# Kernel tuning notes

Measured on AMD Instinct MI355X. Metric: run time of the kernel, lower is better.

The kernel has to match this reference:

```python
import jax, jax.numpy as jnp
import numpy as np

B, K, NP = 2, 48, 25            # batch, context_length, grid_x*grid_y
C, H, L = 768, 12, 6            # n_embd, n_head, n_layer
COLORS, VOCAB, IS = 10, 40, 26  # color_num, vocab_size, intention_size
MAXT = 1000                     # max_timestep
TOK = NP + 4                    # tokens per timestep (rtg, 25 states, action, pnp, intention)
T = K * TOK                     # total sequence length


def layernorm(x, g, b, eps=1e-5):
    m = x.mean(-1, keepdims=True)
    v = ((x - m) ** 2).mean(-1, keepdims=True)
    return (x - m) * jax.lax.rsqrt(v + eps) * g + b


def causal_attn(x, wq, bq, wk, bk, wv, bv, wo, bo):
    Bx, Tx, Cx = x.shape
    hd = Cx // H
    def heads(w, bb):
        return (x @ w + bb).reshape(Bx, Tx, H, hd).transpose(0, 2, 1, 3)
    q, k, v = heads(wq, bq), heads(wk, bk), heads(wv, bv)
    att = jnp.einsum('bhqd,bhkd->bhqk', q, k) * (1.0 / np.sqrt(hd))
    mask = jnp.tril(jnp.ones((Tx, Tx), bool))
    att = jnp.where(mask, att, -jnp.inf)
    att = jax.nn.softmax(att, axis=-1)
    y = jnp.einsum('bhqk,bhkd->bhqd', att, v).transpose(0, 2, 1, 3).reshape(Bx, Tx, Cx)
    return y @ wo + bo


def setup_inputs() -> dict:
    key = jax.random.key(0)
    ks = iter(jax.random.split(key, 64))
    def nrm(shape):
        return jax.random.normal(next(ks), shape, jnp.float32) * 0.02
    inp = dict(
        states=jax.random.randint(next(ks), (B, K * NP), 0, COLORS),
        actions=jax.random.randint(next(ks), (B, K), 0, VOCAB),
        rtgs=jax.random.normal(next(ks), (B, K), jnp.float32),
        timesteps=jax.random.randint(next(ks), (B, K), 0, MAXT + 1),
        pnp=jax.random.normal(next(ks), (B, K, NP), jnp.float32),
        intentions=jax.random.randint(next(ks), (B, K, 2), 0, IS),
        pos_emb=nrm((K + 1, C)),               # (block_size, C)
        global_pos_emb=nrm((MAXT + 1, C)),
        state_tab=nrm((COLORS, C)),
        action_tab=nrm((VOCAB, C)),
        ret_W=nrm((1, C)), ret_b=jnp.zeros((C,)),
        pnp_W=nrm((NP, C)), pnp_b=jnp.zeros((C,)),
        src_tab=nrm((IS, C)), dst_tab=nrm((IS, C)),
        int_W=nrm((2 * C, C)), int_b=jnp.zeros((C,)),
        ln1_g=jnp.ones((L, C)), ln1_b=jnp.zeros((L, C)),
        ln2_g=jnp.ones((L, C)), ln2_b=jnp.zeros((L, C)),
        Wq=nrm((L, C, C)), bq=jnp.zeros((L, C)),
        Wk=nrm((L, C, C)), bk=jnp.zeros((L, C)),
        Wv=nrm((L, C, C)), bv=jnp.zeros((L, C)),
        Wo=nrm((L, C, C)), bo=jnp.zeros((L, C)),
        Wm1=nrm((L, C, 4 * C)), bm1=jnp.zeros((L, 4 * C)),
        Wm2=nrm((L, 4 * C, C)), bm2=jnp.zeros((L, C)),
        lnf_g=jnp.ones((C,)), lnf_b=jnp.zeros((C,)),
        Whs=nrm((C, COLORS)), bhs=jnp.zeros((COLORS,)),
        Wha=nrm((C, VOCAB)), bha=jnp.zeros((VOCAB,)),
        Whr=nrm((C, 1)), bhr=jnp.zeros((1,)),
        Whi=nrm((C, 2 * IS)), bhi=jnp.zeros((2 * IS,)),
    )
    return inp


def reference(states, actions, rtgs, timesteps, pnp, intentions,
              pos_emb, global_pos_emb, state_tab, action_tab,
              ret_W, ret_b, pnp_W, pnp_b, src_tab, dst_tab, int_W, int_b,
              ln1_g, ln1_b, ln2_g, ln2_b, Wq, bq, Wk, bk, Wv, bv, Wo, bo,
              Wm1, bm1, Wm2, bm2, lnf_g, lnf_b,
              Whs, bhs, Wha, bha, Whr, bhr, Whi, bhi):
    # --- embeddings, interleaved as [rtg, state_0..24, action, pnp, intention] per timestep ---
    st = state_tab[states].reshape(B, K, NP, C)                    # strided writes 1+i::TOK
    ae = action_tab[actions][:, :, None, :]
    re = (rtgs[..., None] @ ret_W + ret_b)[:, :, None, :]          # rtgs.unsqueeze(-1) -> Linear(1,C)
    pe = (pnp @ pnp_W + pnp_b)[:, :, None, :]
    ie_in = jnp.concatenate([src_tab[intentions[..., 0]], dst_tab[intentions[..., 1]]], axis=-1)
    ie = (ie_in @ int_W + int_b)[:, :, None, :]
    tok = jnp.concatenate([re, st, ae, pe, ie], axis=2).reshape(B, T, C)
    # --- positions: gather global + local pos_emb[:block_size-1], repeat_interleave by TOK ---
    pos = global_pos_emb[timesteps] + pos_emb[:K][None]            # (B, K, C)
    x = tok + jnp.repeat(pos, TOK, axis=1)
    # --- transformer stack (dropout p=0) ---
    def blk(h, p):
        l1g, l1b, l2g, l2b, wq, bq_, wk, bk_, wv, bv_, wo, bo_, w1, b1, w2, b2 = p
        h = h + causal_attn(layernorm(h, l1g, l1b), wq, bq_, wk, bk_, wv, bv_, wo, bo_)
        m = layernorm(h, l2g, l2b)
        h = h + jax.nn.gelu(m @ w1 + b1, approximate=False) @ w2 + b2
        return h, None
    x, _ = jax.lax.scan(blk, x, (ln1_g, ln1_b, ln2_g, ln2_b, Wq, bq, Wk, bk, Wv, bv, Wo, bo, Wm1, bm1, Wm2, bm2))
    x = layernorm(x, lnf_g, lnf_b)
    xr = x.reshape(B, K, TOK, C)
    logits = x @ Whs + bhs                                         # (B, T, COLORS)
    logit_action = xr[:, :, NP + 1] @ Wha + bha                    # (B, K, VOCAB)
    logit_rtg = (xr[:, :, 0] @ Whr + bhr)[..., 0]                  # (B, K)
    li = xr[:, :, NP + 3] @ Whi + bhi                              # (B, K, 2*IS)
    return logits, logit_action, logit_rtg, li[..., :IS], li[..., IS:]
```

## Files before the change

kernel.cpp:

```cpp
#include <hip/hip_runtime.h>
#include <hip/hip_bf16.h>
#include <math.h>


typedef __hip_bfloat16 bf16;
typedef __attribute__((ext_vector_type(4))) short s4v;
typedef __attribute__((ext_vector_type(8))) short s8v;
typedef __attribute__((ext_vector_type(4))) float f4v;
typedef unsigned int u32;

#define DEV static __device__ __forceinline__

constexpr int NBATCH = 2;
constexpr int NK   = 48;
constexpr int NNP  = 25;
constexpr int NC   = 768;
constexpr int NH   = 12;
constexpr int NL   = 6;
constexpr int NTOK = 29;
constexpr int NT   = NK * NTOK;
constexpr int NM   = NBATCH * NT;
constexpr int MPAD = 2816;

DEV float bs2f(short s) {
  unsigned u = ((unsigned)(unsigned short)s) << 16;
  float f; __builtin_memcpy(&f, &u, 4); return f;
}
DEV short f2bs(float f) {
  bf16 h = __float2bfloat16(f);
  short s; __builtin_memcpy(&s, &h, 2); return s;
}

DEV void async16(const short* g, short* l) {
  __builtin_amdgcn_global_load_lds(
      (const __attribute__((address_space(1))) u32*)g,
      (__attribute__((address_space(3))) u32*)l, 16, 0, 0);
}

__global__ __launch_bounds__(256) void transpose_kernel(
    const float* __restrict__ src, bf16* __restrict__ dst, int R, int C)
{
  int c0 = blockIdx.x * 32, r0 = blockIdx.y * 32;
  __shared__ float tl[32][33];
  int rr = threadIdx.x >> 5, cc = threadIdx.x & 31;
#pragma unroll
  for (int p = 0; p < 4; p++)
    tl[rr + p * 8][cc] = src[(long)(r0 + rr + p * 8) * C + c0 + cc];
  __syncthreads();
#pragma unroll
  for (int p = 0; p < 4; p++)
    dst[(long)(c0 + rr + p * 8) * R + r0 + cc] = __float2bfloat16(tl[cc][rr + p * 8]);
}

__global__ __launch_bounds__(256) void transpose_layer_kernel(
    const float* __restrict__ Wq, const float* __restrict__ Wk,
    const float* __restrict__ Wv, const float* __restrict__ Wo,
    const float* __restrict__ Wm1, const float* __restrict__ Wm2,
    bf16* __restrict__ WqkvT, bf16* __restrict__ WoT,
    bf16* __restrict__ Wm1T, bf16* __restrict__ Wm2T, int multi)
{
  int blk = blockIdx.x;
  int l = blk / 6912, t = blk - l * 6912;
  long so = (long)l * 768 * 768;
  long mo = (long)l * 768 * 3072;
  long dl = multi ? l : 0;
  const float* src; bf16* dst; int R, C, tile;
  if (t < 1728) {
    int m = t / 576; tile = t - m * 576;
    src = (m == 0 ? Wq : (m == 1 ? Wk : Wv)) + so;
    dst = WqkvT + dl * (2304L * 768) + (long)m * 768 * 768; R = 768; C = 768;
  } else if (t < 2304) { src = Wo + so;  dst = WoT  + dl * (768L * 768);  tile = t - 1728; R = 768;  C = 768;  }
  else if (t < 4608)   { src = Wm1 + mo; dst = Wm1T + dl * (3072L * 768); tile = t - 2304; R = 768;  C = 3072; }
  else                 { src = Wm2 + mo; dst = Wm2T + dl * (768L * 3072); tile = t - 4608; R = 3072; C = 768;  }
  int ct = C / 32;
  int tr = tile / ct, tc = tile - tr * ct;
  int r0 = tr * 32, c0 = tc * 32;
  __shared__ float tl[32][33];
  int rr = threadIdx.x >> 5, cc = threadIdx.x & 31;
#pragma unroll
  for (int p = 0; p < 4; p++)
    tl[rr + p * 8][cc] = src[(long)(r0 + rr + p * 8) * C + c0 + cc];
  __syncthreads();
#pragma unroll
  for (int p = 0; p < 4; p++)
    dst[(long)(c0 + rr + p * 8) * R + r0 + cc] = __float2bfloat16(tl[cc][rr + p * 8]);
}

__global__ __launch_bounds__(256) void gather_ie_kernel(
    const int* __restrict__ intentions, const float* __restrict__ src_tab,
    const float* __restrict__ dst_tab, bf16* __restrict__ ie_in)
{
  int idx = blockIdx.x * 256 + threadIdx.x;
  if (idx >= 96 * 1536) return;
  int row = idx / 1536, col = idx - row * 1536;
  float v;
  if (col < 768) v = src_tab[intentions[row * 2 + 0] * 768 + col];
  else           v = dst_tab[intentions[row * 2 + 1] * 768 + col - 768];
  ie_in[idx] = __float2bfloat16(v);
}

__global__ __launch_bounds__(256) void embed_kernel(
    const int* __restrict__ states, const int* __restrict__ actions,
    const float* __restrict__ rtgs, const int* __restrict__ timesteps,
    const float* __restrict__ pnp,
    const float* __restrict__ pos_emb, const float* __restrict__ gpe,
    const float* __restrict__ state_tab, const float* __restrict__ action_tab,
    const float* __restrict__ retW, const float* __restrict__ retb,
    const float* __restrict__ pnpW, const float* __restrict__ pnpb,
    const bf16* __restrict__ ieb, float* __restrict__ X)
{
  int bk = blockIdx.x;
  int b = bk / NK, ts = bk - b * NK;
  int c = blockIdx.y * 256 + threadIdx.x;

  float rtg = rtgs[bk];
  int tstep = timesteps[bk];
  int act   = actions[bk];

  long base = (long)(b * NT + ts * NTOK) * NC;
  float pos = gpe[(long)tstep * NC + c] + pos_emb[ts * NC + c];

  X[base + c] = rtg * retW[c] + retb[c] + pos;
  const int* sp = states + bk * NNP;
#pragma unroll
  for (int i = 0; i < NNP; i++)
    X[base + (1 + i) * NC + c] = state_tab[sp[i] * NC + c] + pos;
  X[base + 26 * NC + c] = action_tab[act * NC + c] + pos;
  float ap = pnpb[c];
  const float* pv = pnp + bk * NNP;
#pragma unroll
  for (int i = 0; i < NNP; i++) ap += pv[i] * pnpW[i * NC + c];
  X[base + 27 * NC + c] = ap + pos;
  X[base + 28 * NC + c] = __bfloat162float(ieb[bk * NC + c]) + pos;
}

__global__ __launch_bounds__(256) void ln_kernel(
    const float* __restrict__ X, bf16* __restrict__ XN,
    const float* __restrict__ g, const float* __restrict__ bt)
{
  int row = blockIdx.x, tid = threadIdx.x;
  const float* x = X + (long)row * NC;
  float v0 = x[tid], v1 = x[tid + 256], v2 = x[tid + 512];
  float s = v0 + v1 + v2;
#pragma unroll
  for (int o = 32; o > 0; o >>= 1) s += __shfl_down(s, o, 64);
  __shared__ float red[8];
  if ((tid & 63) == 0) red[tid >> 6] = s;
  __syncthreads();
  float mean = (red[0] + red[1] + red[2] + red[3]) * (1.0f / NC);
  float d0 = v0 - mean, d1 = v1 - mean, d2 = v2 - mean;
  float qq = d0 * d0 + d1 * d1 + d2 * d2;
#pragma unroll
  for (int o = 32; o > 0; o >>= 1) qq += __shfl_down(qq, o, 64);
  __syncthreads();
  if ((tid & 63) == 0) red[tid >> 6] = qq;
  __syncthreads();
  float var = (red[0] + red[1] + red[2] + red[3]) * (1.0f / NC);
  float rs = 1.0f / sqrtf(var + 1e-5f);
  bf16* xn = XN + (long)row * NC;
  xn[tid      ] = __float2bfloat16(d0 * rs * g[tid      ] + bt[tid      ]);
  xn[tid + 256] = __float2bfloat16(d1 * rs * g[tid + 256] + bt[tid + 256]);
  xn[tid + 512] = __float2bfloat16(d2 * rs * g[tid + 512] + bt[tid + 512]);
}

template<int BM>
__global__ __launch_bounds__(256) void gemm_kernel(
    const bf16* __restrict__ A, const bf16* __restrict__ WT,
    const float* __restrict__ b0, const float* __restrict__ b1,
    const float* __restrict__ b2, int Nsplit,
    bf16* __restrict__ outb, float* __restrict__ resid,
    int M, int N, int K, int flags)
{
  constexpr int IM  = BM / 64;
  constexpr int ACH = BM / 64;
  __shared__ __align__(1024) short As[2][BM * 32];
  __shared__ __align__(1024) short Bs[2][64 * 32];

  int tid = threadIdx.x, wave = tid >> 6, lane = tid & 63;
  int quad = lane >> 4, l16 = lane & 15;
  int m0 = blockIdx.y * BM, n0 = blockIdx.x * 64;
  int wm = wave * (BM / 4);
  int lr = lane >> 2, lc = (lane & 3) * 8;

  const short* Ag = (const short*)A + (long)m0 * K + lc;
  const short* Bg = (const short*)WT + (long)n0 * K + lc;

  const short* ag[ACH]; int alo[ACH];
#pragma unroll
  for (int c = 0; c < ACH; c++) {
    int rbase = wave * (16 * ACH) + c * 16;
    ag[c] = Ag + (long)(rbase + lr) * K;
    alo[c] = rbase * 32;
  }
  const short* bg = Bg + (long)(wave * 16 + lr) * K;
  int blo = wave * 16 * 32;

  f4v zero4 = {0.f, 0.f, 0.f, 0.f};
  f4v acc[IM][4];
#pragma unroll
  for (int i = 0; i < IM; i++)
#pragma unroll
    for (int j = 0; j < 4; j++) acc[i][j] = zero4;

  int nk = K >> 5;
#pragma unroll
  for (int c = 0; c < ACH; c++) async16(ag[c], &As[0][alo[c]]);
  async16(bg, &Bs[0][blo]);
  __syncthreads();

  for (int kt = 0; kt < nk; kt++) {
    int cur = kt & 1, nxt = cur ^ 1;
    if (kt + 1 < nk) {
      int ko = (kt + 1) << 5;
#pragma unroll
      for (int c = 0; c < ACH; c++) async16(ag[c] + ko, &As[nxt][alo[c]]);
      async16(bg + ko, &Bs[nxt][blo]);
    }
    s8v af[IM], bf8[4];
#pragma unroll
    for (int i = 0; i < IM; i++) {
      const short* p = &As[cur][(wm + i * 16 + l16) * 32 + quad * 8];
      af[i].lo = *(const s4v*)p; af[i].hi = *(const s4v*)(p + 4);
    }
#pragma unroll
    for (int j = 0; j < 4; j++) {
      const short* p = &Bs[cur][(j * 16 + l16) * 32 + quad * 8];
      bf8[j].lo = *(const s4v*)p; bf8[j].hi = *(const s4v*)(p + 4);
    }
#pragma unroll
    for (int i = 0; i < IM; i++)
#pragma unroll
      for (int j = 0; j < 4; j++)
        acc[i][j] = __builtin_amdgcn_mfma_f32_16x16x32_bf16(af[i], bf8[j], acc[i][j], 0, 0, 0);
    __syncthreads();
  }

#pragma unroll
  for (int i = 0; i < IM; i++) {
    int rbase = m0 + wm + i * 16 + quad * 4;
#pragma unroll
    for (int j = 0; j < 4; j++) {
      int bc = n0 + j * 16;
      int wsel = bc / Nsplit;
      const float* bp = wsel == 0 ? b0 : (wsel == 1 ? b1 : b2);
      float bv = bp[bc - wsel * Nsplit + l16];
      int col = bc + l16;
#pragma unroll
      for (int r = 0; r < 4; r++) {
        int row = rbase + r;
        if (row < M) {
          float v = acc[i][j][r] + bv;
          if (flags & 1) v = 0.5f * v * (1.0f + erff(v * 0.70710678118654752f));
          if (flags & 2) resid[(long)row * N + col] += v;
          else outb[(long)row * N + col] = __float2bfloat16(v);
        }
      }
    }
  }
}

constexpr int ASTR = 72;

__global__ __launch_bounds__(256) void attn_kernel(
    const bf16* __restrict__ QKV, bf16* __restrict__ Yg)
{
  int qt = blockIdx.x, h = blockIdx.y, b = blockIdx.z;
  int q0 = qt * 64;
  int tid = threadIdx.x, wave = tid >> 6, lane = tid & 63, quad = lane >> 4, l16 = lane & 15;

  __shared__ short Qs[64 * ASTR];
  __shared__ short Ks[64 * ASTR];
  __shared__ short Vt[64 * ASTR];
  __shared__ short Ps[64 * ASTR];
  __shared__ float S[64 * 65];
  __shared__ float mrow[64], lrow[64], arow[64];
  __shared__ float red[256];

  if (tid < 64) { mrow[tid] = -1e30f; lrow[tid] = 0.f; }

  int r = tid >> 2, c16 = (tid & 3) * 16;
  const short* src = (const short*)QKV;
  s8v zz = {0,0,0,0,0,0,0,0};

  s8v qv0 = zz, qv1 = zz;
  if (q0 + r < NT) {
    const s8v* p = (const s8v*)(src + (long)(b * NT + q0 + r) * 2304 + h * 64 + c16);
    qv0 = p[0]; qv1 = p[1];
  }
  {
    short* qp = &Qs[r * ASTR + c16];
    *(s4v*)(qp    ) = qv0.lo; *(s4v*)(qp + 4) = qv0.hi;
    *(s4v*)(qp + 8) = qv1.lo; *(s4v*)(qp + 12) = qv1.hi;
  }

  f4v zero4 = {0.f, 0.f, 0.f, 0.f};
  f4v Of[4];
#pragma unroll
  for (int j = 0; j < 4; j++) Of[j] = zero4;

  int kend = q0 + 63; if (kend > NT - 1) kend = NT - 1;
  for (int k0 = 0; k0 <= kend; k0 += 64) {
    s8v kv0 = zz, kv1 = zz, vv0 = zz, vv1 = zz;
    if (k0 + r < NT) {
      const s8v* pk = (const s8v*)(src + (long)(b * NT + k0 + r) * 2304 + 768 + h * 64 + c16);
      kv0 = pk[0]; kv1 = pk[1];
      const s8v* pvv = (const s8v*)(src + (long)(b * NT + k0 + r) * 2304 + 1536 + h * 64 + c16);
      vv0 = pvv[0]; vv1 = pvv[1];
    }
    __syncthreads();
    {
      short* kp = &Ks[r * ASTR + c16];
      *(s4v*)(kp    ) = kv0.lo; *(s4v*)(kp + 4) = kv0.hi;
      *(s4v*)(kp + 8) = kv1.lo; *(s4v*)(kp + 12) = kv1.hi;
      short* vt = &Vt[c16 * ASTR + r];
      vt[ 0 * ASTR] = vv0.s0; vt[ 1 * ASTR] = vv0.s1; vt[ 2 * ASTR] = vv0.s2; vt[ 3 * ASTR] = vv0.s3;
      vt[ 4 * ASTR] = vv0.s4; vt[ 5 * ASTR] = vv0.s5; vt[ 6 * ASTR] = vv0.s6; vt[ 7 * ASTR] = vv0.s7;
      vt[ 8 * ASTR] = vv1.s0; vt[ 9 * ASTR] = vv1.s1; vt[10 * ASTR] = vv1.s2; vt[11 * ASTR] = vv1.s3;
      vt[12 * ASTR] = vv1.s4; vt[13 * ASTR] = vv1.s5; vt[14 * ASTR] = vv1.s6; vt[15 * ASTR] = vv1.s7;
    }
    __syncthreads();

    f4v sa[4];
#pragma unroll
    for (int j = 0; j < 4; j++) sa[j] = zero4;
#pragma unroll
    for (int ks = 0; ks < 2; ks++) {
      const short* pa = &Qs[(wave * 16 + l16) * ASTR + ks * 32 + quad * 8];
      s8v aq; aq.lo = *(const s4v*)pa; aq.hi = *(const s4v*)(pa + 4);
#pragma unroll
      for (int j = 0; j < 4; j++) {
        const short* pb = &Ks[(j * 16 + l16) * ASTR + ks * 32 + quad * 8];
        s8v bk8; bk8.lo = *(const s4v*)pb; bk8.hi = *(const s4v*)(pb + 4);
        sa[j] = __builtin_amdgcn_mfma_f32_16x16x32_bf16(aq, bk8, sa[j], 0, 0, 0);
      }
    }
#pragma unroll
    for (int j = 0; j < 4; j++) {
#pragma unroll
      for (int rg = 0; rg < 4; rg++) {
        int rloc = wave * 16 + quad * 4 + rg;
        int cloc = j * 16 + l16;
        int gq = q0 + rloc, gk = k0 + cloc;
        float sv = (gk <= gq && gq < NT) ? sa[j][rg] * 0.125f : -1e30f;
        S[rloc * 65 + cloc] = sv;
      }
    }
    __syncthreads();

    float mx = -1e30f;
#pragma unroll
    for (int c = 0; c < 16; c++) mx = fmaxf(mx, S[r * 65 + c16 + c]);
    red[r * 4 + (tid & 3)] = mx;
    __syncthreads();
    if (tid < 64) {
      float tm = fmaxf(fmaxf(red[tid * 4], red[tid * 4 + 1]), fmaxf(red[tid * 4 + 2], red[tid * 4 + 3]));
      float mn = fmaxf(mrow[tid], tm);
      arow[tid] = __expf(mrow[tid] - mn);
      mrow[tid] = mn;
    }
    __syncthreads();

    float mr = mrow[r];
    float psum = 0.f;
#pragma unroll
    for (int c = 0; c < 16; c++) {
      float e = __expf(S[r * 65 + c16 + c] - mr);
      psum += e;
      Ps[r * ASTR + c16 + c] = f2bs(e);
    }
    red[r * 4 + (tid & 3)] = psum;
    __syncthreads();
    if (tid < 64)
      lrow[tid] = lrow[tid] * arow[tid] + red[tid * 4] + red[tid * 4 + 1] + red[tid * 4 + 2] + red[tid * 4 + 3];
#pragma unroll
    for (int j = 0; j < 4; j++)
#pragma unroll
      for (int rg = 0; rg < 4; rg++)
        Of[j][rg] *= arow[wave * 16 + quad * 4 + rg];
    __syncthreads();

#pragma unroll
    for (int ks = 0; ks < 2; ks++) {
      const short* pa = &Ps[(wave * 16 + l16) * ASTR + ks * 32 + quad * 8];
      s8v ap8; ap8.lo = *(const s4v*)pa; ap8.hi = *(const s4v*)(pa + 4);
#pragma unroll
      for (int j = 0; j < 4; j++) {
        const short* pb = &Vt[(j * 16 + l16) * ASTR + ks * 32 + quad * 8];
        s8v vp8; vp8.lo = *(const s4v*)pb; vp8.hi = *(const s4v*)(pb + 4);
        Of[j] = __builtin_amdgcn_mfma_f32_16x16x32_bf16(ap8, vp8, Of[j], 0, 0, 0);
      }
    }
  }
  __syncthreads();
#pragma unroll
  for (int j = 0; j < 4; j++) {
#pragma unroll
    for (int rg = 0; rg < 4; rg++) {
      int rloc = wave * 16 + quad * 4 + rg;
      int gq = q0 + rloc;
      if (gq < NT) {
        float ov = Of[j][rg] / lrow[rloc];
        Yg[(long)(b * NT + gq) * NC + h * 64 + j * 16 + l16] = __float2bfloat16(ov);
      }
    }
  }
}

__global__ __launch_bounds__(256) void head_logits_kernel(
    const bf16* __restrict__ XN, const float* __restrict__ Whs,
    const float* __restrict__ bhs, float* __restrict__ out)
{
  int idx = blockIdx.x * 256 + threadIdx.x;
  if (idx >= NM * 10) return;
  int row = idx / 10, n = idx - row * 10;
  const short* x = (const short*)XN + (long)row * NC;
  float a0 = bhs[n], a1 = 0.f, a2 = 0.f, a3 = 0.f;
  for (int k = 0; k < NC; k += 4) {
    a0 += bs2f(x[k    ]) * Whs[(k    ) * 10 + n];
    a1 += bs2f(x[k + 1]) * Whs[(k + 1) * 10 + n];
    a2 += bs2f(x[k + 2]) * Whs[(k + 2) * 10 + n];
    a3 += bs2f(x[k + 3]) * Whs[(k + 3) * 10 + n];
  }
  out[idx] = a0 + a1 + a2 + a3;
}

__global__ __launch_bounds__(128) void head_small_kernel(
    const bf16* __restrict__ XN,
    const float* __restrict__ Wha, const float* __restrict__ bha,
    const float* __restrict__ Whr, const float* __restrict__ bhr,
    const float* __restrict__ Whi, const float* __restrict__ bhi,
    float* __restrict__ outA, float* __restrict__ outR,
    float* __restrict__ outS, float* __restrict__ outD)
{
  int blk = blockIdx.x;
  int b = blk / NK, ts = blk - b * NK;
  int tid = threadIdx.x;
  if (tid >= 93) return;
  const short* xs = (const short*)XN;
  if (tid < 40) {
    long row = (long)(b * NT + ts * NTOK + 26) * NC;
    float a0 = bha[tid], a1 = 0.f, a2 = 0.f, a3 = 0.f;
    for (int k = 0; k < NC; k += 4) {
      a0 += bs2f(xs[row + k    ]) * Wha[(k    ) * 40 + tid];
      a1 += bs2f(xs[row + k + 1]) * Wha[(k + 1) * 40 + tid];
      a2 += bs2f(xs[row + k + 2]) * Wha[(k + 2) * 40 + tid];
      a3 += bs2f(xs[row + k + 3]) * Wha[(k + 3) * 40 + tid];
    }
    outA[blk * 40 + tid] = a0 + a1 + a2 + a3;
  } else if (tid == 40) {
    long row = (long)(b * NT + ts * NTOK) * NC;
    float a0 = bhr[0], a1 = 0.f, a2 = 0.f, a3 = 0.f;
    for (int k = 0; k < NC; k += 4) {
      a0 += bs2f(xs[row + k    ]) * Whr[k    ];
      a1 += bs2f(xs[row + k + 1]) * Whr[k + 1];
      a2 += bs2f(xs[row + k + 2]) * Whr[k + 2];
      a3 += bs2f(xs[row + k + 3]) * Whr[k + 3];
    }
    outR[blk] = a0 + a1 + a2 + a3;
  } else {
    int n = tid - 41;
    long row = (long)(b * NT + ts * NTOK + 28) * NC;
    float a0 = bhi[n], a1 = 0.f, a2 = 0.f, a3 = 0.f;
    for (int k = 0; k < NC; k += 4) {
      a0 += bs2f(xs[row + k    ]) * Whi[(k    ) * 52 + n];
      a1 += bs2f(xs[row + k + 1]) * Whi[(k + 1) * 52 + n];
      a2 += bs2f(xs[row + k + 2]) * Whi[(k + 2) * 52 + n];
      a3 += bs2f(xs[row + k + 3]) * Whi[(k + 3) * 52 + n];
    }
    if (n < 26) outS[blk * 26 + n] = a0 + a1 + a2 + a3;
    else        outD[blk * 26 + (n - 26)] = a0 + a1 + a2 + a3;
  }
}

extern "C" void kernel_launch(void* const* d_in, const int* in_sizes, int n_in,
                              void* d_out, int out_size, void* d_ws, size_t ws_size,
                              hipStream_t stream)
{
  (void)in_sizes; (void)n_in; (void)out_size;

  const int*   states     = (const int*)  d_in[0];
  const int*   actions    = (const int*)  d_in[1];
  const float* rtgs       = (const float*)d_in[2];
  const int*   timesteps  = (const int*)  d_in[3];
  const float* pnp        = (const float*)d_in[4];
  const int*   intentions = (const int*)  d_in[5];
  const float* pos_emb    = (const float*)d_in[6];
  const float* gpe        = (const float*)d_in[7];
  const float* state_tab  = (const float*)d_in[8];
  const float* action_tab = (const float*)d_in[9];
  const float* retW  = (const float*)d_in[10];
  const float* retb  = (const float*)d_in[11];
  const float* pnpW  = (const float*)d_in[12];
  const float* pnpb  = (const float*)d_in[13];
  const float* src_tab = (const float*)d_in[14];
  const float* dst_tab = (const float*)d_in[15];
  const float* intW  = (const float*)d_in[16];
  const float* intb  = (const float*)d_in[17];
  const float* ln1g  = (const float*)d_in[18];
  const float* ln1b  = (const float*)d_in[19];
  const float* ln2g  = (const float*)d_in[20];
  const float* ln2b  = (const float*)d_in[21];
  const float* Wq = (const float*)d_in[22];
  const float* bq = (const float*)d_in[23];
  const float* Wk = (const float*)d_in[24];
  const float* bk = (const float*)d_in[25];
  const float* Wv = (const float*)d_in[26];
  const float* bv = (const float*)d_in[27];
  const float* Wo = (const float*)d_in[28];
  const float* bo = (const float*)d_in[29];
  const float* Wm1 = (const float*)d_in[30];
  const float* bm1 = (const float*)d_in[31];
  const float* Wm2 = (const float*)d_in[32];
  const float* bm2 = (const float*)d_in[33];
  const float* lnfg = (const float*)d_in[34];
  const float* lnfb = (const float*)d_in[35];
  const float* Whs = (const float*)d_in[36];
  const float* bhs = (const float*)d_in[37];
  const float* Wha = (const float*)d_in[38];
  const float* bha = (const float*)d_in[39];
  const float* Whr = (const float*)d_in[40];
  const float* bhr = (const float*)d_in[41];
  const float* Whi = (const float*)d_in[42];
  const float* bhi = (const float*)d_in[43];

  char* wsb = (char*)d_ws;
  float* X   = (float*)(wsb);
  bf16* XN   = (bf16*)(wsb + 8650752);
  bf16* QKVb = (bf16*)(wsb + 12976128);
  bf16* Yb   = (bf16*)(wsb + 25952256);
  bf16* H1   = QKVb;
  bf16* WTbase = (bf16*)(wsb + 30277632);

  const size_t NEED_BIG = 30277632UL + 84934656UL + 2949120UL;
  bool big = ws_size >= NEED_BIG;

  long sQKV = 2304L * 768, sO = 768L * 768, sM1 = 3072L * 768, sM2 = 768L * 3072;
  bf16 *WqkvT, *WoT, *Wm1T, *Wm2T, *intWT;
  if (big) {
    WqkvT = WTbase;
    WoT   = WqkvT + 6 * sQKV;
    Wm1T  = WoT   + 6 * sO;
    Wm2T  = Wm1T  + 6 * sM1;
    intWT = Wm2T  + 6 * sM2;
  } else {
    WqkvT = WTbase;
    WoT   = WqkvT + sQKV;
    Wm1T  = WoT + sO;
    Wm2T  = Wm1T + sM1;
    intWT = WTbase;
  }
  bf16* ie_in = intWT + 768L * 1536;
  bf16* ieb   = ie_in + 128L * 1536;

  float* out0 = (float*)d_out;
  float* out1 = out0 + 27840;
  float* out2 = out1 + 3840;
  float* out3 = out2 + 96;
  float* out4 = out3 + 2496;

  transpose_kernel<<<dim3(24, 48), 256, 0, stream>>>(intW, intWT, 1536, 768);
  gather_ie_kernel<<<(96 * 1536 + 255) / 256, 256, 0, stream>>>(intentions, src_tab, dst_tab, ie_in);
  gemm_kernel<64><<<dim3(12, 2), 256, 0, stream>>>(ie_in, intWT, intb, intb, intb, 768,
      ieb, nullptr, 96, 768, 1536, 0);
  embed_kernel<<<dim3(96, 3), 256, 0, stream>>>(
      states, actions, rtgs, timesteps, pnp, pos_emb, gpe, state_tab, action_tab,
      retW, retb, pnpW, pnpb, ieb, X);

  if (big)
    transpose_layer_kernel<<<6912 * NL, 256, 0, stream>>>(
        Wq, Wk, Wv, Wo, Wm1, Wm2, WqkvT, WoT, Wm1T, Wm2T, 1);

  for (int l = 0; l < NL; l++) {
    const long wofs = (long)l * NC * NC;
    const long mofs = (long)l * NC * 4 * NC;
    if (!big)
      transpose_layer_kernel<<<6912, 256, 0, stream>>>(
          Wq + wofs, Wk + wofs, Wv + wofs, Wo + wofs, Wm1 + mofs, Wm2 + mofs,
          WqkvT, WoT, Wm1T, Wm2T, 0);
    bf16* wqkv = big ? WqkvT + l * sQKV : WqkvT;
    bf16* wo   = big ? WoT   + l * sO   : WoT;
    bf16* wm1  = big ? Wm1T  + l * sM1  : Wm1T;
    bf16* wm2  = big ? Wm2T  + l * sM2  : Wm2T;

    ln_kernel<<<NM, 256, 0, stream>>>(X, XN, ln1g + l * NC, ln1b + l * NC);
    gemm_kernel<128><<<dim3(36, 22), 256, 0, stream>>>(XN, wqkv,
        bq + l * NC, bk + l * NC, bv + l * NC, 768, QKVb, nullptr, NM, 2304, NC, 0);
    attn_kernel<<<dim3(22, NH, NBATCH), 256, 0, stream>>>(QKVb, Yb);
    gemm_kernel<64><<<dim3(12, 44), 256, 0, stream>>>(Yb, wo,
        bo + l * NC, bo + l * NC, bo + l * NC, 768, nullptr, X, NM, 768, NC, 2);
    ln_kernel<<<NM, 256, 0, stream>>>(X, XN, ln2g + l * NC, ln2b + l * NC);
    gemm_kernel<128><<<dim3(48, 22), 256, 0, stream>>>(XN, wm1,
        bm1 + l * 4 * NC, bm1 + l * 4 * NC, bm1 + l * 4 * NC, 4 * NC, H1, nullptr,
        NM, 3072, NC, 1);
    gemm_kernel<64><<<dim3(12, 44), 256, 0, stream>>>(H1, wm2,
        bm2 + l * NC, bm2 + l * NC, bm2 + l * NC, 768, nullptr, X, NM, 768, 4 * NC, 2);
  }
  ln_kernel<<<NM, 256, 0, stream>>>(X, XN, lnfg, lnfb);
  head_logits_kernel<<<(NM * 10 + 255) / 256, 256, 0, stream>>>(XN, Whs, bhs, out0);
  head_small_kernel<<<NBATCH * NK, 128, 0, stream>>>(XN, Wha, bha, Whr, bhr, Whi, bhi,
      out1, out2, out3, out4);
}
```

Baseline: 1.627 ms.

## Widen GEMM N-tile to 128 for QKV/MLP1 and vectorize weight transpose

Parameterizes the GEMM kernel by an N-tile width, so the QKV and MLP-up projections use 128x128 tiles and each A tile is reused across more output columns. This cuts redundant global/LDS traffic per FLOP, at the cost of more accumulator registers and fewer blocks (396 and 528), which may lower occupancy. The weight transpose kernel also switches to 64x64 tiles with float4 loads, bf16 staging in LDS, and 8-byte stores, reducing the block count and memory transactions of the per-call fp32-to-bf16 weight conversion.

```diff
diff --git a/kernel.cpp b/kernel.cpp
--- a/kernel.cpp
+++ b/kernel.cpp
@@ -60,30 +60,40 @@
     bf16* __restrict__ Wm1T, bf16* __restrict__ Wm2T, int multi)
 {
   int blk = blockIdx.x;
-  int l = blk / 6912, t = blk - l * 6912;
+  int l = blk / 1728, t = blk - l * 1728;
   long so = (long)l * 768 * 768;
   long mo = (long)l * 768 * 3072;
   long dl = multi ? l : 0;
   const float* src; bf16* dst; int R, C, tile;
-  if (t < 1728) {
-    int m = t / 576; tile = t - m * 576;
+  if (t < 432) {
+    int m = t / 144; tile = t - m * 144;
     src = (m == 0 ? Wq : (m == 1 ? Wk : Wv)) + so;
     dst = WqkvT + dl * (2304L * 768) + (long)m * 768 * 768; R = 768; C = 768;
-  } else if (t < 2304) { src = Wo + so;  dst = WoT  + dl * (768L * 768);  tile = t - 1728; R = 768;  C = 768;  }
-  else if (t < 4608)   { src = Wm1 + mo; dst = Wm1T + dl * (3072L * 768); tile = t - 2304; R = 768;  C = 3072; }
-  else                 { src = Wm2 + mo; dst = Wm2T + dl * (768L * 3072); tile = t - 4608; R = 3072; C = 768;  }
-  int ct = C / 32;
+  } else if (t < 576)  { src = Wo + so;  dst = WoT  + dl * (768L * 768);  tile = t - 432;  R = 768;  C = 768;  }
+  else if (t < 1152)   { src = Wm1 + mo; dst = Wm1T + dl * (3072L * 768); tile = t - 576;  R = 768;  C = 3072; }
+  else                 { src = Wm2 + mo; dst = Wm2T + dl * (768L * 3072); tile = t - 1152; R = 3072; C = 768;  }
+  int ct = C / 64;
   int tr = tile / ct, tc = tile - tr * ct;
-  int r0 = tr * 32, c0 = tc * 32;
-  __shared__ float tl[32][33];
-  int rr = threadIdx.x >> 5, cc = threadIdx.x & 31;
-#pragma unroll
-  for (int p = 0; p < 4; p++)
-    tl[rr + p * 8][cc] = src[(long)(r0 + rr + p * 8) * C + c0 + cc];
+  int r0 = tr * 64, c0 = tc * 64;
+
+  __shared__ short tl[64][66];
+  int t4 = threadIdx.x & 15, rr = threadIdx.x >> 4;
+#pragma unroll
+  for (int p = 0; p < 4; p++) {
+    int row = rr + p * 16;
+    f4v v = *(const f4v*)(src + (long)(r0 + row) * C + c0 + t4 * 4);
+    tl[t4 * 4 + 0][row] = f2bs(v.x);
+    tl[t4 * 4 + 1][row] = f2bs(v.y);
+    tl[t4 * 4 + 2][row] = f2bs(v.z);
+    tl[t4 * 4 + 3][row] = f2bs(v.w);
+  }
   __syncthreads();
 #pragma unroll
-  for (int p = 0; p < 4; p++)
-    dst[(long)(c0 + rr + p * 8) * R + r0 + cc] = __float2bfloat16(tl[cc][rr + p * 8]);
+  for (int p = 0; p < 4; p++) {
+    int drow = rr + p * 16;
+    s4v w = *(const s4v*)&tl[drow][t4 * 4];
+    *(s4v*)((short*)dst + (long)(c0 + drow) * R + r0 + t4 * 4) = w;
+  }
 }
 
 __global__ __launch_bounds__(256) void gather_ie_kernel(
@@ -163,7 +173,7 @@
   xn[tid + 512] = __float2bfloat16(d2 * rs * g[tid + 512] + bt[tid + 512]);
 }
 
-template<int BM>
+template<int BM, int BN>
 __global__ __launch_bounds__(256) void gemm_kernel(
     const bf16* __restrict__ A, const bf16* __restrict__ WT,
     const float* __restrict__ b0, const float* __restrict__ b1,
@@ -172,13 +182,15 @@
     int M, int N, int K, int flags)
 {
   constexpr int IM  = BM / 64;
+  constexpr int JN  = BN / 16;
   constexpr int ACH = BM / 64;
+  constexpr int BCH = BN / 64;
   __shared__ __align__(1024) short As[2][BM * 32];
-  __shared__ __align__(1024) short Bs[2][64 * 32];
+  __shared__ __align__(1024) short Bs[2][BN * 32];
 
   int tid = threadIdx.x, wave = tid >> 6, lane = tid & 63;
   int quad = lane >> 4, l16 = lane & 15;
-  int m0 = blockIdx.y * BM, n0 = blockIdx.x * 64;
+  int m0 = blockIdx.y * BM, n0 = blockIdx.x * BN;
   int wm = wave * (BM / 4);
   int lr = lane >> 2, lc = (lane & 3) * 8;
 
@@ -192,20 +204,26 @@
     ag[c] = Ag + (long)(rbase + lr) * K;
     alo[c] = rbase * 32;
   }
-  const short* bg = Bg + (long)(wave * 16 + lr) * K;
-  int blo = wave * 16 * 32;
+  const short* bg[BCH]; int blo[BCH];
+#pragma unroll
+  for (int c = 0; c < BCH; c++) {
+    int rbase = wave * (16 * BCH) + c * 16;
+    bg[c] = Bg + (long)(rbase + lr) * K;
+    blo[c] = rbase * 32;
+  }
 
   f4v zero4 = {0.f, 0.f, 0.f, 0.f};
-  f4v acc[IM][4];
+  f4v acc[IM][JN];
 #pragma unroll
   for (int i = 0; i < IM; i++)
 #pragma unroll
-    for (int j = 0; j < 4; j++) acc[i][j] = zero4;
+    for (int j = 0; j < JN; j++) acc[i][j] = zero4;
 
   int nk = K >> 5;
 #pragma unroll
   for (int c = 0; c < ACH; c++) async16(ag[c], &As[0][alo[c]]);
-  async16(bg, &Bs[0][blo]);
+#pragma unroll
+  for (int c = 0; c < BCH; c++) async16(bg[c], &Bs[0][blo[c]]);
   __syncthreads();
 
   for (int kt = 0; kt < nk; kt++) {
@@ -214,23 +232,24 @@
       int ko = (kt + 1) << 5;
 #pragma unroll
       for (int c = 0; c < ACH; c++) async16(ag[c] + ko, &As[nxt][alo[c]]);
-      async16(bg + ko, &Bs[nxt][blo]);
-    }
-    s8v af[IM], bf8[4];
+#pragma unroll
+      for (int c = 0; c < BCH; c++) async16(bg[c] + ko, &Bs[nxt][blo[c]]);
+    }
+    s8v af[IM], bf8[JN];
 #pragma unroll
     for (int i = 0; i < IM; i++) {
       const short* p = &As[cur][(wm + i * 16 + l16) * 32 + quad * 8];
       af[i].lo = *(const s4v*)p; af[i].hi = *(const s4v*)(p + 4);
     }
 #pragma unroll
-    for (int j = 0; j < 4; j++) {
+    for (int j = 0; j < JN; j++) {
       const short* p = &Bs[cur][(j * 16 + l16) * 32 + quad * 8];
       bf8[j].lo = *(const s4v*)p; bf8[j].hi = *(const s4v*)(p + 4);
     }
 #pragma unroll
     for (int i = 0; i < IM; i++)
 #pragma unroll
-      for (int j = 0; j < 4; j++)
+      for (int j = 0; j < JN; j++)
         acc[i][j] = __builtin_amdgcn_mfma_f32_16x16x32_bf16(af[i], bf8[j], acc[i][j], 0, 0, 0);
     __syncthreads();
   }
@@ -239,7 +258,7 @@
   for (int i = 0; i < IM; i++) {
     int rbase = m0 + wm + i * 16 + quad * 4;
 #pragma unroll
-    for (int j = 0; j < 4; j++) {
+    for (int j = 0; j < JN; j++) {
       int bc = n0 + j * 16;
       int wsel = bc / Nsplit;
       const float* bp = wsel == 0 ? b0 : (wsel == 1 ? b1 : b2);
@@ -560,21 +579,21 @@
 
   transpose_kernel<<<dim3(24, 48), 256, 0, stream>>>(intW, intWT, 1536, 768);
   gather_ie_kernel<<<(96 * 1536 + 255) / 256, 256, 0, stream>>>(intentions, src_tab, dst_tab, ie_in);
-  gemm_kernel<64><<<dim3(12, 2), 256, 0, stream>>>(ie_in, intWT, intb, intb, intb, 768,
+  gemm_kernel<64, 64><<<dim3(12, 2), 256, 0, stream>>>(ie_in, intWT, intb, intb, intb, 768,
       ieb, nullptr, 96, 768, 1536, 0);
   embed_kernel<<<dim3(96, 3), 256, 0, stream>>>(
       states, actions, rtgs, timesteps, pnp, pos_emb, gpe, state_tab, action_tab,
       retW, retb, pnpW, pnpb, ieb, X);
 
   if (big)
-    transpose_layer_kernel<<<6912 * NL, 256, 0, stream>>>(
+    transpose_layer_kernel<<<1728 * NL, 256, 0, stream>>>(
         Wq, Wk, Wv, Wo, Wm1, Wm2, WqkvT, WoT, Wm1T, Wm2T, 1);
 
   for (int l = 0; l < NL; l++) {
     const long wofs = (long)l * NC * NC;
     const long mofs = (long)l * NC * 4 * NC;
     if (!big)
-      transpose_layer_kernel<<<6912, 256, 0, stream>>>(
+      transpose_layer_kernel<<<1728, 256, 0, stream>>>(
           Wq + wofs, Wk + wofs, Wv + wofs, Wo + wofs, Wm1 + mofs, Wm2 + mofs,
           WqkvT, WoT, Wm1T, Wm2T, 0);
     bf16* wqkv = big ? WqkvT + l * sQKV : WqkvT;
@@ -583,16 +602,16 @@
     bf16* wm2  = big ? Wm2T  + l * sM2  : Wm2T;
 
     ln_kernel<<<NM, 256, 0, stream>>>(X, XN, ln1g + l * NC, ln1b + l * NC);
-    gemm_kernel<128><<<dim3(36, 22), 256, 0, stream>>>(XN, wqkv,
+    gemm_kernel<128, 128><<<dim3(18, 22), 256, 0, stream>>>(XN, wqkv,
         bq + l * NC, bk + l * NC, bv + l * NC, 768, QKVb, nullptr, NM, 2304, NC, 0);
     attn_kernel<<<dim3(22, NH, NBATCH), 256, 0, stream>>>(QKVb, Yb);
-    gemm_kernel<64><<<dim3(12, 44), 256, 0, stream>>>(Yb, wo,
+    gemm_kernel<64, 64><<<dim3(12, 44), 256, 0, stream>>>(Yb, wo,
         bo + l * NC, bo + l * NC, bo + l * NC, 768, nullptr, X, NM, 768, NC, 2);
     ln_kernel<<<NM, 256, 0, stream>>>(X, XN, ln2g + l * NC, ln2b + l * NC);
-    gemm_kernel<128><<<dim3(48, 22), 256, 0, stream>>>(XN, wm1,
+    gemm_kernel<128, 128><<<dim3(24, 22), 256, 0, stream>>>(XN, wm1,
         bm1 + l * 4 * NC, bm1 + l * 4 * NC, bm1 + l * 4 * NC, 4 * NC, H1, nullptr,
         NM, 3072, NC, 1);
-    gemm_kernel<64><<<dim3(12, 44), 256, 0, stream>>>(H1, wm2,
+    gemm_kernel<64, 64><<<dim3(12, 44), 256, 0, stream>>>(H1, wm2,
         bm2 + l * NC, bm2 + l * NC, bm2 + l * NC, 768, nullptr, X, NM, 768, 4 * NC, 2);
   }
   ln_kernel<<<NM, 256, 0, stream>>>(X, XN, lnfg, lnfb);
```

Measured after the change: 1.680 ms. 1.03x slower.
